# Kernel optimization log

Measured on AMD Instinct MI355X. Metric: run time of the kernel, lower is better.

## Reference

```python
import jax, jax.numpy as jnp
import numpy as np

B, NA, NAA, NPC = 8, 4096, 1024, 4096
K, KNC, G, DA, F, D = 16, 14, 32, 12, 128, 128
NCAT = 38
EPS = 1e-5


def _bgather(x, idx):
    # per-batch fancy gather: x [B, N, ...], idx [B, ...] -> x[b, idx[b]]
    return jax.vmap(lambda a, i: a[i])(x, idx)


def _normalize(v):
    return v / (jnp.linalg.norm(v, axis=-1, keepdims=True) + 1e-8)


def setup_inputs() -> dict:
    key = jax.random.key(0)
    ks = jax.random.split(key, 12)
    return {
        'point_clouds': jax.random.normal(ks[0], (B, NPC, 3), jnp.float32),
        'mask_atom': jnp.ones((B, NA, 1), jnp.float32),
        'mask_aa': jnp.ones((B, NAA, 1), jnp.float32),
        'attr_table': jax.random.normal(ks[1], (NCAT + 1, DA), jnp.float32) * 0.1,
        'gauss_centers': jax.random.normal(ks[2], (G, 3), jnp.float32),
        'W_nem': jax.random.normal(ks[3], (G, DA, F), jnp.float32) / np.sqrt(G * DA),
        'W_att': jax.random.normal(ks[4], (F, D), jnp.float32) / np.sqrt(F),
        'W_feat': jax.random.normal(ks[5], (F, D), jnp.float32) / np.sqrt(F),
        'bn_gamma': jnp.ones((D,), jnp.float32),
        'bn_beta': jnp.zeros((D,), jnp.float32),
        'frame_idx': jax.random.randint(ks[6], (B, NA, 3), 0, NPC),
        'attr_idx': jax.random.randint(ks[7], (B, NA), 0, NCAT + 1),
        'nb_idx': jax.random.randint(ks[8], (B, NA, K), 0, NA),
        'seq_idx_atom': jnp.sort(jax.random.randint(ks[9], (B, NA), 0, NAA), axis=-1),
        'seq_idx_aa': jnp.sort(jax.random.randint(ks[10], (B, NAA), 0, NAA), axis=-1),
        'aa_nb_idx': jax.random.randint(ks[11], (B, NAA, KNC), 0, NA),
    }


def reference(point_clouds, mask_atom, mask_aa, attr_table, gauss_centers,
              W_nem, W_att, W_feat, bn_gamma, bn_beta,
              frame_idx, attr_idx, nb_idx, seq_idx_atom, seq_idx_aa, aa_nb_idx):
    # --- frame builder: local orthonormal frame per atom from 3 gathered points ---
    pts = _bgather(point_clouds, frame_idx)          # [B,NA,3,3]
    center = pts[:, :, 1, :]                         # [B,NA,3]
    u1 = _normalize(pts[:, :, 2, :] - center)
    v = pts[:, :, 0, :] - center
    u2 = _normalize(v - jnp.sum(v * u1, -1, keepdims=True) * u1)
    u3 = jnp.cross(u1, u2)
    R = jnp.stack([u1, u2, u3], axis=-2)             # [B,NA,3,3] rows = axes

    # --- attribute embedding + derived mask (mattr = any nonzero along embed dim) ---
    a = attr_table[attr_idx]                         # [B,NA,DA]
    mattr = jnp.any(a != 0, axis=-1, keepdims=True).astype(a.dtype)
    mask_y = mask_atom * mattr                       # [B,NA,1]

    # --- neighborhood embedding: gather K neighbors, local coords, gaussian basis ---
    c_nb = _bgather(center, nb_idx)                  # [B,NA,K,3]
    rel = jnp.einsum('bnij,bnkj->bnki', R, c_nb - center[:, :, None, :])
    d2 = jnp.sum((rel[:, :, :, None, :] - gauss_centers) ** 2, -1)   # [B,NA,K,G]
    g = jnp.exp(-0.5 * d2)
    a_nb = _bgather(a * mattr, nb_idx)               # [B,NA,K,DA]
    y = jnp.einsum('bnkg,bnka,gaf->bnf', g, a_nb, W_nem) / K          # [B,NA,F]
    y = y * mask_y

    # --- pooling projections (bias-free linears), repeated mask multiplies ---
    att = (y @ W_att) * mask_y                       # [B,NA,D] (one head per channel)
    feat = (y @ W_feat) * mask_y                     # [B,NA,D]

    # --- Neighborhood_Computation: gather 14 atoms per amino acid ---
    att_l = _bgather(att, aa_nb_idx)                 # [B,NAA,KNC,D]
    feat_l = _bgather(feat, aa_nb_idx)               # [B,NAA,KNC,D]
    mask_nb = _bgather(mask_y, aa_nb_idx)            # [B,NAA,KNC,1]
    seq_nb = _bgather(seq_idx_atom, aa_nb_idx)       # [B,NAA,KNC]
    indice_diff = jnp.clip(jnp.abs(seq_nb - seq_idx_aa[:, :, None]), 0, 1).astype(att_l.dtype)
    gate = (1.0 - indice_diff)[..., None]            # pool_mask = 1 - indice_diff

    # --- attention pooling over the 14-neighborhood, gated + masked softmax ---
    logits = jnp.where(mask_nb > 0, att_l, -1e9)
    w = jax.nn.softmax(logits, axis=2) * gate * mask_nb
    w = w / (jnp.sum(w, axis=2, keepdims=True) + 1e-8)
    pooled = jnp.sum(w * feat_l, axis=2) * mask_aa   # [B,NAA,D]

    # --- masked BatchNorm1d over valid aa positions, then ReLU ---
    n = jnp.sum(mask_aa) + 1e-8
    mean = jnp.sum(pooled * mask_aa, (0, 1)) / n
    var = jnp.sum(mask_aa * (pooled - mean) ** 2, (0, 1)) / n
    out = bn_gamma * (pooled - mean) * jax.lax.rsqrt(var + EPS) + bn_beta
    out = jax.nn.relu(out * mask_aa)
    return out, mask_aa
```

## Files before the change

### kernel.cpp

```cpp
#include <hip/hip_runtime.h>
#include <hip/hip_bf16.h>

#define B_    8
#define NA_   4096
#define NAA_  1024
#define NPC_  4096
#define K_    16
#define KNC_  14
#define G_    32
#define DA_   12
#define F_    128
#define D_    128

typedef __attribute__((ext_vector_type(8))) short short8;
typedef __attribute__((ext_vector_type(4))) float floatx4;

__device__ __forceinline__ unsigned short f2bf(float x) {
    __hip_bfloat16 h = __float2bfloat16(x);
    return *reinterpret_cast<unsigned short*>(&h);
}
__device__ __forceinline__ float bf2f(unsigned short u) {
    __hip_bfloat16 h;
    *reinterpret_cast<unsigned short*>(&h) = u;
    return __bfloat162float(h);
}

__global__ __launch_bounds__(256) void k_geom(
    const float* __restrict__ pc,
    const float* __restrict__ mask_atom,
    const float* __restrict__ attr_table,
    const float* __restrict__ gauss,
    const int* __restrict__ frame_idx,
    const int* __restrict__ attr_idx,
    const int* __restrict__ nb_idx,
    const float* __restrict__ W_nem, const float* __restrict__ W_att,
    const float* __restrict__ W_feat,
    unsigned int* __restrict__ Mout,
    float* __restrict__ mask_y,
    unsigned short* __restrict__ WnT,
    unsigned short* __restrict__ W2T)
{
    const int tid = threadIdx.x;

    if (blockIdx.x >= 4096) {
        const int idx = (blockIdx.x - 4096) * 256 + tid;
        if (idx < 128 * 384) {
            const int f = idx / 384, ga = idx % 384;
            WnT[idx] = f2bf(W_nem[(size_t)ga * F_ + f]);
        } else if (idx < 128 * 384 + 256 * 128) {
            const int j = idx - 128 * 384;
            const int n = j / 128, k = j % 128;
            const float v = (n < 128) ? W_att[(size_t)k * F_ + n]
                                      : W_feat[(size_t)k * F_ + (n - 128)];
            W2T[j] = f2bf(v);
        }
        return;
    }

    const int a0 = blockIdx.x * 8;
    const int b  = a0 >> 12;

    __shared__ float  Rs[8][9];
    __shared__ float  cen[8][3];
    __shared__ int    nbs[8][K_];
    __shared__ int    ais[8][K_];
    __shared__ __align__(16) float rel4[8][K_][4];
    __shared__ __align__(16) float anb4[8][K_][12];

    if (tid < 8) {
        const int atom = a0 + tid;
        const int fb = atom * 3;
        const int i0 = frame_idx[fb + 0];
        const int i1 = frame_idx[fb + 1];
        const int i2 = frame_idx[fb + 2];
        const float* pcb = pc + (size_t)b * NPC_ * 3;
        float p0x = pcb[i0*3+0], p0y = pcb[i0*3+1], p0z = pcb[i0*3+2];
        float cx  = pcb[i1*3+0], cy  = pcb[i1*3+1], cz  = pcb[i1*3+2];
        float p2x = pcb[i2*3+0], p2y = pcb[i2*3+1], p2z = pcb[i2*3+2];
        float u1x = p2x - cx, u1y = p2y - cy, u1z = p2z - cz;
        float n1 = sqrtf(u1x*u1x + u1y*u1y + u1z*u1z) + 1e-8f;
        u1x /= n1; u1y /= n1; u1z /= n1;
        float vx = p0x - cx, vy = p0y - cy, vz = p0z - cz;
        float dot = vx*u1x + vy*u1y + vz*u1z;
        float u2x = vx - dot*u1x, u2y = vy - dot*u1y, u2z = vz - dot*u1z;
        float n2 = sqrtf(u2x*u2x + u2y*u2y + u2z*u2z) + 1e-8f;
        u2x /= n2; u2y /= n2; u2z /= n2;
        float u3x = u1y*u2z - u1z*u2y;
        float u3y = u1z*u2x - u1x*u2z;
        float u3z = u1x*u2y - u1y*u2x;
        Rs[tid][0]=u1x; Rs[tid][1]=u1y; Rs[tid][2]=u1z;
        Rs[tid][3]=u2x; Rs[tid][4]=u2y; Rs[tid][5]=u2z;
        Rs[tid][6]=u3x; Rs[tid][7]=u3y; Rs[tid][8]=u3z;
        cen[tid][0]=cx; cen[tid][1]=cy; cen[tid][2]=cz;
        const int ai = attr_idx[atom];
        float m = 0.f;
        #pragma unroll
        for (int a = 0; a < DA_; a++)
            if (attr_table[ai*DA_ + a] != 0.f) m = 1.f;
        mask_y[atom] = mask_atom[atom] * m;
    }
    if (tid < 128) {
        const int t = tid >> 4, k = tid & 15;
        nbs[t][k] = nb_idx[(a0 + t) * K_ + k];
    }
    __syncthreads();

    if (tid < 128) {
        const int t = tid >> 4, k = tid & 15;
        const int j  = nbs[t][k];
        ais[t][k] = attr_idx[b * NA_ + j];
        const int fj = frame_idx[(b * NA_ + j) * 3 + 1];
        const float* pcb = pc + (size_t)b * NPC_ * 3;
        float dx = pcb[fj*3+0] - cen[t][0];
        float dy = pcb[fj*3+1] - cen[t][1];
        float dz = pcb[fj*3+2] - cen[t][2];
        rel4[t][k][0] = Rs[t][0]*dx + Rs[t][1]*dy + Rs[t][2]*dz;
        rel4[t][k][1] = Rs[t][3]*dx + Rs[t][4]*dy + Rs[t][5]*dz;
        rel4[t][k][2] = Rs[t][6]*dx + Rs[t][7]*dy + Rs[t][8]*dz;
        rel4[t][k][3] = 0.f;
    }
    __syncthreads();

    if (tid < 128) {
        const int t = tid >> 4, k = tid & 15;
        const float4* src = (const float4*)attr_table + (size_t)ais[t][k] * 3;
        float4* dst = (float4*)&anb4[t][k][0];
        dst[0] = src[0]; dst[1] = src[1]; dst[2] = src[2];
    }
    __syncthreads();

    {
        const int t = tid >> 5, g = tid & 31;
        const float gx = gauss[g*3+0], gy = gauss[g*3+1], gz = gauss[g*3+2];
        float acc[DA_];
        #pragma unroll
        for (int a = 0; a < DA_; a++) acc[a] = 0.f;
        #pragma unroll
        for (int k = 0; k < K_; k++) {
            const float4 r  = *(const float4*)&rel4[t][k][0];
            const float dx = r.x - gx, dy = r.y - gy, dz = r.z - gz;
            const float gv = __expf(-0.5f * (dx*dx + dy*dy + dz*dz));
            const float4 a0 = *(const float4*)&anb4[t][k][0];
            const float4 a1 = *(const float4*)&anb4[t][k][4];
            const float4 a2 = *(const float4*)&anb4[t][k][8];
            acc[0] += gv*a0.x; acc[1] += gv*a0.y; acc[2] += gv*a0.z; acc[3] += gv*a0.w;
            acc[4] += gv*a1.x; acc[5] += gv*a1.y; acc[6] += gv*a1.z; acc[7] += gv*a1.w;
            acc[8] += gv*a2.x; acc[9] += gv*a2.y; acc[10]+= gv*a2.z; acc[11]+= gv*a2.w;
        }
        const int atom = a0 + t;
        unsigned int* dst = Mout + (size_t)atom * (384/2) + g * 6;
        #pragma unroll
        for (int i = 0; i < 6; i++) {
            const unsigned int lo = f2bf(acc[2*i]);
            const unsigned int hi = f2bf(acc[2*i+1]);
            dst[i] = lo | (hi << 16);
        }
    }
}

__global__ __launch_bounds__(256) void k_gemm(
    const unsigned short* __restrict__ M,
    const unsigned short* __restrict__ WnT,
    const unsigned short* __restrict__ W2T,
    const float* __restrict__ masky,
    unsigned short* __restrict__ AF)
{
    const int mb   = blockIdx.x * 32;
    const int wave = threadIdx.x >> 6, lane = threadIdx.x & 63;
    const int l15  = lane & 15, quad = lane >> 4;

    __shared__ __align__(16) unsigned short Ys[32][136];
    __shared__ float mk[32];

    if (threadIdx.x < 32) mk[threadIdx.x] = masky[mb + threadIdx.x];

    const int n0 = wave * 32;
    const unsigned short* ap0 = M   + (size_t)(mb + l15) * 384 + quad * 8;
    const unsigned short* ap1 = ap0 + (size_t)16 * 384;
    const unsigned short* bp0 = WnT + (size_t)(n0 + l15) * 384 + quad * 8;
    const unsigned short* bp1 = bp0 + (size_t)16 * 384;

    floatx4 c00 = {0.f,0.f,0.f,0.f}, c01 = {0.f,0.f,0.f,0.f};
    floatx4 c10 = {0.f,0.f,0.f,0.f}, c11 = {0.f,0.f,0.f,0.f};
    #pragma unroll
    for (int k0 = 0; k0 < 384; k0 += 32) {
        short8 a0 = *reinterpret_cast<const short8*>(ap0 + k0);
        short8 a1 = *reinterpret_cast<const short8*>(ap1 + k0);
        short8 b0 = *reinterpret_cast<const short8*>(bp0 + k0);
        short8 b1 = *reinterpret_cast<const short8*>(bp1 + k0);
        c00 = __builtin_amdgcn_mfma_f32_16x16x32_bf16(a0, b0, c00, 0, 0, 0);
        c01 = __builtin_amdgcn_mfma_f32_16x16x32_bf16(a0, b1, c01, 0, 0, 0);
        c10 = __builtin_amdgcn_mfma_f32_16x16x32_bf16(a1, b0, c10, 0, 0, 0);
        c11 = __builtin_amdgcn_mfma_f32_16x16x32_bf16(a1, b1, c11, 0, 0, 0);
    }
    __syncthreads();
    #pragma unroll
    for (int r = 0; r < 4; r++) {
        const int r0 = quad * 4 + r;
        const float s0 = mk[r0]      * (1.f / 16.f);
        const float s1 = mk[16 + r0] * (1.f / 16.f);
        Ys[r0][n0 + l15]           = f2bf(c00[r] * s0);
        Ys[r0][n0 + 16 + l15]      = f2bf(c01[r] * s0);
        Ys[16 + r0][n0 + l15]      = f2bf(c10[r] * s1);
        Ys[16 + r0][n0 + 16 + l15] = f2bf(c11[r] * s1);
    }
    __syncthreads();

    const int c0 = wave * 64;
    const unsigned short* bq = W2T + (size_t)(c0 + l15) * F_ + quad * 8;

    floatx4 f0[4], f1[4];
    #pragma unroll
    for (int t = 0; t < 4; t++) {
        f0[t] = (floatx4){0.f,0.f,0.f,0.f};
        f1[t] = (floatx4){0.f,0.f,0.f,0.f};
    }
    #pragma unroll
    for (int k0 = 0; k0 < 128; k0 += 32) {
        short8 a0 = *reinterpret_cast<const short8*>(&Ys[l15][k0 + quad * 8]);
        short8 a1 = *reinterpret_cast<const short8*>(&Ys[16 + l15][k0 + quad * 8]);
        #pragma unroll
        for (int t = 0; t < 4; t++) {
            short8 b = *reinterpret_cast<const short8*>(bq + (size_t)t * 16 * F_ + k0);
            f0[t] = __builtin_amdgcn_mfma_f32_16x16x32_bf16(a0, b, f0[t], 0, 0, 0);
            f1[t] = __builtin_amdgcn_mfma_f32_16x16x32_bf16(a1, b, f1[t], 0, 0, 0);
        }
    }
    #pragma unroll
    for (int r = 0; r < 4; r++) {
        const int r0 = quad * 4 + r;
        const float s0 = mk[r0], s1 = mk[16 + r0];
        unsigned short* o0 = AF + (size_t)(mb + r0) * 256 + c0 + l15;
        unsigned short* o1 = AF + (size_t)(mb + 16 + r0) * 256 + c0 + l15;
        #pragma unroll
        for (int t = 0; t < 4; t++) {
            o0[t * 16] = f2bf(f0[t][r] * s0);
            o1[t * 16] = f2bf(f1[t][r] * s1);
        }
    }
}

__global__ __launch_bounds__(256) void k_pool(
    const unsigned short* __restrict__ AF,
    const float* __restrict__ mask_y,
    const float* __restrict__ mask_aa,
    const int* __restrict__ seq_idx_atom,
    const int* __restrict__ seq_idx_aa,
    const int* __restrict__ aa_nb_idx,
    float* __restrict__ pooled)
{
    const int tid = threadIdx.x;
    const int rl  = tid >> 7;
    const int f   = tid & 127;
    const int row = blockIdx.x * 2 + rl;
    const int b   = row >> 10;

    __shared__ float gateS[2][KNC_], maskS[2][KNC_];
    __shared__ int   jS[2][KNC_];

    if (tid < 2 * KNC_) {
        const int r = tid / KNC_, k = tid % KNC_;
        const int rr = blockIdx.x * 2 + r;
        const int j = aa_nb_idx[rr * KNC_ + k];
        jS[r][k] = j;
        maskS[r][k] = mask_y[(rr >> 10) * NA_ + j];
        const int sa = seq_idx_aa[rr];
        const int sn = seq_idx_atom[(rr >> 10) * NA_ + j];
        gateS[r][k] = (sn == sa) ? 1.f : 0.f;
    }
    __syncthreads();

    float av[KNC_], fv[KNC_];
    #pragma unroll
    for (int k = 0; k < KNC_; k++) {
        const size_t o = ((size_t)(b * NA_ + jS[rl][k])) * 256 + f;
        av[k] = bf2f(AF[o]);
        fv[k] = bf2f(AF[o + 128]);
    }
    float m = -1e30f;
    #pragma unroll
    for (int k = 0; k < KNC_; k++) {
        const float l = (maskS[rl][k] > 0.f) ? av[k] : -1e9f;
        av[k] = l;
        m = fmaxf(m, l);
    }
    float s = 0.f;
    #pragma unroll
    for (int k = 0; k < KNC_; k++) { av[k] = __expf(av[k] - m); s += av[k]; }
    float tot = 0.f, p = 0.f;
    #pragma unroll
    for (int k = 0; k < KNC_; k++) {
        const float w = av[k] / s * gateS[rl][k] * maskS[rl][k];
        tot += w;
        p   += w * fv[k];
    }
    p = p / (tot + 1e-8f);
    p *= mask_aa[row];
    pooled[(size_t)row * F_ + f] = p;
}

__global__ __launch_bounds__(128) void k_stats(
    const float* __restrict__ pooled,
    const float* __restrict__ mask_aa,
    float* __restrict__ stats)
{
    const int tid = threadIdx.x;
    const int r0  = blockIdx.x * 128;
    float s1 = 0.f, s2 = 0.f;
    for (int r = 0; r < 128; r++) {
        const float v = pooled[(size_t)(r0 + r) * F_ + tid];
        s1 += v;
        s2 += v * v;
    }
    atomicAdd(&stats[tid], s1);
    atomicAdd(&stats[F_ + tid], s2);
    if (tid == 0) {
        float n = 0.f;
        for (int r = 0; r < 128; r++) n += mask_aa[r0 + r];
        atomicAdd(&stats[2 * F_], n);
    }
}

__global__ __launch_bounds__(256) void k_final(
    const float* __restrict__ pooled,
    const float* __restrict__ stats,
    const float* __restrict__ gamma,
    const float* __restrict__ beta,
    const float* __restrict__ mask_aa,
    float* __restrict__ out)
{
    const int idx = blockIdx.x * 256 + threadIdx.x;
    const int f   = idx & (D_ - 1);
    const int row = idx >> 7;
    const float n    = stats[2 * F_] + 1e-8f;
    const float mean = stats[f] / n;
    const float var  = stats[F_ + f] / n - mean * mean;
    const float ma   = mask_aa[row];
    float v = gamma[f] * (pooled[idx] - mean) * rsqrtf(var + 1e-5f) + beta[f];
    v = fmaxf(v * ma, 0.f);
    out[idx] = v;
    if (idx < B_ * NAA_) out[B_ * NAA_ * D_ + idx] = mask_aa[idx];
}

extern "C" void kernel_launch(void* const* d_in, const int* in_sizes, int n_in,
                              void* d_out, int out_size, void* d_ws, size_t ws_size,
                              hipStream_t stream) {
    const float* pc         = (const float*)d_in[0];
    const float* mask_atom  = (const float*)d_in[1];
    const float* mask_aa    = (const float*)d_in[2];
    const float* attr_table = (const float*)d_in[3];
    const float* gauss      = (const float*)d_in[4];
    const float* W_nem      = (const float*)d_in[5];
    const float* W_att      = (const float*)d_in[6];
    const float* W_feat     = (const float*)d_in[7];
    const float* gamma      = (const float*)d_in[8];
    const float* beta       = (const float*)d_in[9];
    const int* frame_idx    = (const int*)d_in[10];
    const int* attr_idx     = (const int*)d_in[11];
    const int* nb_idx       = (const int*)d_in[12];
    const int* seq_idx_atom = (const int*)d_in[13];
    const int* seq_idx_aa   = (const int*)d_in[14];
    const int* aa_nb_idx    = (const int*)d_in[15];

    char* base = (char*)d_ws;
    unsigned short* M   = (unsigned short*)base;
    unsigned short* AF  = (unsigned short*)(base + 25165824);
    unsigned short* WnT = (unsigned short*)(base + 25165824 + 16777216);
    unsigned short* W2T = (unsigned short*)(base + 25165824 + 16777216 + 98304);
    float* masky  = (float*)(base + 25165824 + 16777216 + 98304 + 65536);
    float* pooled = (float*)(base + 25165824 + 16777216 + 98304 + 65536 + 131072);
    float* stats  = (float*)(base + 25165824 + 16777216 + 98304 + 65536 + 131072 + 4194304);

    hipMemsetAsync(stats, 0, 257 * sizeof(float), stream);

    k_geom<<<4096 + 320, 256, 0, stream>>>(pc, mask_atom, attr_table, gauss,
                                           frame_idx, attr_idx, nb_idx,
                                           W_nem, W_att, W_feat,
                                           (unsigned int*)M, masky, WnT, W2T);
    k_gemm<<<B_*NA_/32, 256, 0, stream>>>(M, WnT, W2T, masky, AF);
    k_pool<<<B_*NAA_/2, 256, 0, stream>>>(AF, masky, mask_aa,
                                          seq_idx_atom, seq_idx_aa, aa_nb_idx,
                                          pooled);
    k_stats<<<64, 128, 0, stream>>>(pooled, mask_aa, stats);
    k_final<<<(B_*NAA_*D_) / 256, 256, 0, stream>>>(pooled, stats, gamma, beta,
                                                    mask_aa, (float*)d_out);
}
```

Measured before the change: 171.7 us.

## Fuse geometry+GEMM via shared-memory M tile and fold BN stats into pooling

The weight-transpose prep moves into its own small kernel. The geometry/Gaussian-embedding stage is merged with the MFMA GEMM so the 32x384 bf16 M tile stays in LDS instead of round-tripping about 25 MB through global memory. Attribute neighbours are stored as packed bf16 in LDS, and the geometry scratch shares space with the GEMM's Ys buffer. The pooling kernel now handles 8 rows per block and accumulates the BatchNorm sums with a block reduction, which removes the separate serial stats kernel. The risks are lower occupancy from the larger LDS footprint and small precision changes from storing attributes as bf16.

```diff
diff --git a/kernel.cpp b/kernel.cpp
--- a/kernel.cpp
+++ b/kernel.cpp
@@ -24,8 +24,32 @@
     *reinterpret_cast<unsigned short*>(&h) = u;
     return __bfloat162float(h);
 }
-
-__global__ __launch_bounds__(256) void k_geom(
+__device__ __forceinline__ float bflo(unsigned int u) {
+    return __uint_as_float(u << 16);
+}
+__device__ __forceinline__ float bfhi(unsigned int u) {
+    return __uint_as_float(u & 0xffff0000u);
+}
+
+__global__ __launch_bounds__(256) void k_prep(
+    const float* __restrict__ W_nem, const float* __restrict__ W_att,
+    const float* __restrict__ W_feat,
+    unsigned short* __restrict__ WnT, unsigned short* __restrict__ W2T)
+{
+    const int idx = blockIdx.x * 256 + threadIdx.x;
+    if (idx < 128 * 384) {
+        const int f = idx / 384, ga = idx % 384;
+        WnT[idx] = f2bf(W_nem[(size_t)ga * F_ + f]);
+    } else if (idx < 128 * 384 + 256 * 128) {
+        const int j = idx - 128 * 384;
+        const int n = j / 128, k = j % 128;
+        const float v = (n < 128) ? W_att[(size_t)k * F_ + n]
+                                  : W_feat[(size_t)k * F_ + (n - 128)];
+        W2T[j] = f2bf(v);
+    }
+}
+
+__global__ __launch_bounds__(256, 3) void k_fused(
     const float* __restrict__ pc,
     const float* __restrict__ mask_atom,
     const float* __restrict__ attr_table,
@@ -33,41 +57,28 @@
     const int* __restrict__ frame_idx,
     const int* __restrict__ attr_idx,
     const int* __restrict__ nb_idx,
-    const float* __restrict__ W_nem, const float* __restrict__ W_att,
-    const float* __restrict__ W_feat,
-    unsigned int* __restrict__ Mout,
+    const unsigned short* __restrict__ WnT,
+    const unsigned short* __restrict__ W2T,
     float* __restrict__ mask_y,
-    unsigned short* __restrict__ WnT,
-    unsigned short* __restrict__ W2T)
+    unsigned short* __restrict__ AF)
 {
+    const int a0  = blockIdx.x * 32;
+    const int b   = a0 >> 12;
     const int tid = threadIdx.x;
-
-    if (blockIdx.x >= 4096) {
-        const int idx = (blockIdx.x - 4096) * 256 + tid;
-        if (idx < 128 * 384) {
-            const int f = idx / 384, ga = idx % 384;
-            WnT[idx] = f2bf(W_nem[(size_t)ga * F_ + f]);
-        } else if (idx < 128 * 384 + 256 * 128) {
-            const int j = idx - 128 * 384;
-            const int n = j / 128, k = j % 128;
-            const float v = (n < 128) ? W_att[(size_t)k * F_ + n]
-                                      : W_feat[(size_t)k * F_ + (n - 128)];
-            W2T[j] = f2bf(v);
-        }
-        return;
-    }
-
-    const int a0 = blockIdx.x * 8;
-    const int b  = a0 >> 12;
-
-    __shared__ float  Rs[8][9];
-    __shared__ float  cen[8][3];
-    __shared__ int    nbs[8][K_];
-    __shared__ int    ais[8][K_];
-    __shared__ __align__(16) float rel4[8][K_][4];
-    __shared__ __align__(16) float anb4[8][K_][12];
-
-    if (tid < 8) {
+    const int wave = tid >> 6, lane = tid & 63;
+    const int l15 = lane & 15, quad = lane >> 4;
+
+    __shared__ unsigned short Ms[32][392];
+    __shared__ __align__(16) char geo_union[20480];
+    __shared__ float Rs[32][9];
+    __shared__ float cen[32][3];
+    __shared__ float mk[32];
+
+    float4        (*rel4)[K_]    = (float4(*)[K_])geo_union;
+    unsigned int  (*anbP)[K_][6] = (unsigned int(*)[K_][6])(geo_union + 8192);
+    unsigned short(*Ys)[136]     = (unsigned short(*)[136])geo_union;
+
+    if (tid < 32) {
         const int atom = a0 + tid;
         const int fb = atom * 3;
         const int i0 = frame_idx[fb + 0];
@@ -97,58 +108,60 @@
         #pragma unroll
         for (int a = 0; a < DA_; a++)
             if (attr_table[ai*DA_ + a] != 0.f) m = 1.f;
-        mask_y[atom] = mask_atom[atom] * m;
-    }
-    if (tid < 128) {
-        const int t = tid >> 4, k = tid & 15;
-        nbs[t][k] = nb_idx[(a0 + t) * K_ + k];
-    }
-    __syncthreads();
-
-    if (tid < 128) {
-        const int t = tid >> 4, k = tid & 15;
-        const int j  = nbs[t][k];
-        ais[t][k] = attr_idx[b * NA_ + j];
+        const float mv = mask_atom[atom] * m;
+        mk[tid] = mv;
+        mask_y[atom] = mv;
+    }
+    __syncthreads();
+
+    #pragma unroll
+    for (int it = 0; it < 2; it++) {
+        const int idx = tid + it * 256;
+        const int t = idx >> 4, k = idx & 15;
+        const int j  = nb_idx[(a0 + t) * K_ + k];
+        const int ai = attr_idx[b * NA_ + j];
         const int fj = frame_idx[(b * NA_ + j) * 3 + 1];
         const float* pcb = pc + (size_t)b * NPC_ * 3;
         float dx = pcb[fj*3+0] - cen[t][0];
         float dy = pcb[fj*3+1] - cen[t][1];
         float dz = pcb[fj*3+2] - cen[t][2];
-        rel4[t][k][0] = Rs[t][0]*dx + Rs[t][1]*dy + Rs[t][2]*dz;
-        rel4[t][k][1] = Rs[t][3]*dx + Rs[t][4]*dy + Rs[t][5]*dz;
-        rel4[t][k][2] = Rs[t][6]*dx + Rs[t][7]*dy + Rs[t][8]*dz;
-        rel4[t][k][3] = 0.f;
-    }
-    __syncthreads();
-
-    if (tid < 128) {
-        const int t = tid >> 4, k = tid & 15;
-        const float4* src = (const float4*)attr_table + (size_t)ais[t][k] * 3;
-        float4* dst = (float4*)&anb4[t][k][0];
-        dst[0] = src[0]; dst[1] = src[1]; dst[2] = src[2];
-    }
-    __syncthreads();
-
-    {
-        const int t = tid >> 5, g = tid & 31;
+        float4 r;
+        r.x = Rs[t][0]*dx + Rs[t][1]*dy + Rs[t][2]*dz;
+        r.y = Rs[t][3]*dx + Rs[t][4]*dy + Rs[t][5]*dz;
+        r.z = Rs[t][6]*dx + Rs[t][7]*dy + Rs[t][8]*dz;
+        r.w = 0.f;
+        rel4[t][k] = r;
+        const float4* src = (const float4*)attr_table + (size_t)ai * 3;
+        #pragma unroll
+        for (int q = 0; q < 3; q++) {
+            const float4 v = src[q];
+            anbP[t][k][q*2]   = (unsigned int)f2bf(v.x) | ((unsigned int)f2bf(v.y) << 16);
+            anbP[t][k][q*2+1] = (unsigned int)f2bf(v.z) | ((unsigned int)f2bf(v.w) << 16);
+        }
+    }
+    __syncthreads();
+
+    #pragma unroll
+    for (int it = 0; it < 4; it++) {
+        const int idx = tid + it * 256;
+        const int t = idx >> 5, g = idx & 31;
         const float gx = gauss[g*3+0], gy = gauss[g*3+1], gz = gauss[g*3+2];
         float acc[DA_];
         #pragma unroll
         for (int a = 0; a < DA_; a++) acc[a] = 0.f;
         #pragma unroll
         for (int k = 0; k < K_; k++) {
-            const float4 r  = *(const float4*)&rel4[t][k][0];
+            const float4 r = rel4[t][k];
             const float dx = r.x - gx, dy = r.y - gy, dz = r.z - gz;
             const float gv = __expf(-0.5f * (dx*dx + dy*dy + dz*dz));
-            const float4 a0 = *(const float4*)&anb4[t][k][0];
-            const float4 a1 = *(const float4*)&anb4[t][k][4];
-            const float4 a2 = *(const float4*)&anb4[t][k][8];
-            acc[0] += gv*a0.x; acc[1] += gv*a0.y; acc[2] += gv*a0.z; acc[3] += gv*a0.w;
-            acc[4] += gv*a1.x; acc[5] += gv*a1.y; acc[6] += gv*a1.z; acc[7] += gv*a1.w;
-            acc[8] += gv*a2.x; acc[9] += gv*a2.y; acc[10]+= gv*a2.z; acc[11]+= gv*a2.w;
-        }
-        const int atom = a0 + t;
-        unsigned int* dst = Mout + (size_t)atom * (384/2) + g * 6;
+            #pragma unroll
+            for (int q = 0; q < 6; q++) {
+                const unsigned int u = anbP[t][k][q];
+                acc[2*q]   += gv * bflo(u);
+                acc[2*q+1] += gv * bfhi(u);
+            }
+        }
+        unsigned int* dst = (unsigned int*)&Ms[t][g * 12];
         #pragma unroll
         for (int i = 0; i < 6; i++) {
             const unsigned int lo = f2bf(acc[2*i]);
@@ -156,27 +169,9 @@
             dst[i] = lo | (hi << 16);
         }
     }
-}
-
-__global__ __launch_bounds__(256) void k_gemm(
-    const unsigned short* __restrict__ M,
-    const unsigned short* __restrict__ WnT,
-    const unsigned short* __restrict__ W2T,
-    const float* __restrict__ masky,
-    unsigned short* __restrict__ AF)
-{
-    const int mb   = blockIdx.x * 32;
-    const int wave = threadIdx.x >> 6, lane = threadIdx.x & 63;
-    const int l15  = lane & 15, quad = lane >> 4;
-
-    __shared__ __align__(16) unsigned short Ys[32][136];
-    __shared__ float mk[32];
-
-    if (threadIdx.x < 32) mk[threadIdx.x] = masky[mb + threadIdx.x];
+    __syncthreads();
 
     const int n0 = wave * 32;
-    const unsigned short* ap0 = M   + (size_t)(mb + l15) * 384 + quad * 8;
-    const unsigned short* ap1 = ap0 + (size_t)16 * 384;
     const unsigned short* bp0 = WnT + (size_t)(n0 + l15) * 384 + quad * 8;
     const unsigned short* bp1 = bp0 + (size_t)16 * 384;
 
@@ -184,14 +179,14 @@
     floatx4 c10 = {0.f,0.f,0.f,0.f}, c11 = {0.f,0.f,0.f,0.f};
     #pragma unroll
     for (int k0 = 0; k0 < 384; k0 += 32) {
-        short8 a0 = *reinterpret_cast<const short8*>(ap0 + k0);
-        short8 a1 = *reinterpret_cast<const short8*>(ap1 + k0);
+        short8 a0v = *reinterpret_cast<const short8*>(&Ms[l15][quad * 8 + k0]);
+        short8 a1v = *reinterpret_cast<const short8*>(&Ms[16 + l15][quad * 8 + k0]);
         short8 b0 = *reinterpret_cast<const short8*>(bp0 + k0);
         short8 b1 = *reinterpret_cast<const short8*>(bp1 + k0);
-        c00 = __builtin_amdgcn_mfma_f32_16x16x32_bf16(a0, b0, c00, 0, 0, 0);
-        c01 = __builtin_amdgcn_mfma_f32_16x16x32_bf16(a0, b1, c01, 0, 0, 0);
-        c10 = __builtin_amdgcn_mfma_f32_16x16x32_bf16(a1, b0, c10, 0, 0, 0);
-        c11 = __builtin_amdgcn_mfma_f32_16x16x32_bf16(a1, b1, c11, 0, 0, 0);
+        c00 = __builtin_amdgcn_mfma_f32_16x16x32_bf16(a0v, b0, c00, 0, 0, 0);
+        c01 = __builtin_amdgcn_mfma_f32_16x16x32_bf16(a0v, b1, c01, 0, 0, 0);
+        c10 = __builtin_amdgcn_mfma_f32_16x16x32_bf16(a1v, b0, c10, 0, 0, 0);
+        c11 = __builtin_amdgcn_mfma_f32_16x16x32_bf16(a1v, b1, c11, 0, 0, 0);
     }
     __syncthreads();
     #pragma unroll
@@ -217,21 +212,21 @@
     }
     #pragma unroll
     for (int k0 = 0; k0 < 128; k0 += 32) {
-        short8 a0 = *reinterpret_cast<const short8*>(&Ys[l15][k0 + quad * 8]);
-        short8 a1 = *reinterpret_cast<const short8*>(&Ys[16 + l15][k0 + quad * 8]);
+        short8 a0v = *reinterpret_cast<const short8*>(&Ys[l15][k0 + quad * 8]);
+        short8 a1v = *reinterpret_cast<const short8*>(&Ys[16 + l15][k0 + quad * 8]);
         #pragma unroll
         for (int t = 0; t < 4; t++) {
-            short8 b = *reinterpret_cast<const short8*>(bq + (size_t)t * 16 * F_ + k0);
-            f0[t] = __builtin_amdgcn_mfma_f32_16x16x32_bf16(a0, b, f0[t], 0, 0, 0);
-            f1[t] = __builtin_amdgcn_mfma_f32_16x16x32_bf16(a1, b, f1[t], 0, 0, 0);
+            short8 bv = *reinterpret_cast<const short8*>(bq + (size_t)t * 16 * F_ + k0);
+            f0[t] = __builtin_amdgcn_mfma_f32_16x16x32_bf16(a0v, bv, f0[t], 0, 0, 0);
+            f1[t] = __builtin_amdgcn_mfma_f32_16x16x32_bf16(a1v, bv, f1[t], 0, 0, 0);
         }
     }
     #pragma unroll
     for (int r = 0; r < 4; r++) {
         const int r0 = quad * 4 + r;
         const float s0 = mk[r0], s1 = mk[16 + r0];
-        unsigned short* o0 = AF + (size_t)(mb + r0) * 256 + c0 + l15;
-        unsigned short* o1 = AF + (size_t)(mb + 16 + r0) * 256 + c0 + l15;
+        unsigned short* o0 = AF + (size_t)(a0 + r0) * 256 + c0 + l15;
+        unsigned short* o1 = AF + (size_t)(a0 + 16 + r0) * 256 + c0 + l15;
         #pragma unroll
         for (int t = 0; t < 4; t++) {
             o0[t * 16] = f2bf(f0[t][r] * s0);
@@ -240,83 +235,87 @@
     }
 }
 
-__global__ __launch_bounds__(256) void k_pool(
+__global__ __launch_bounds__(256) void k_pool_stats(
     const unsigned short* __restrict__ AF,
     const float* __restrict__ mask_y,
     const float* __restrict__ mask_aa,
     const int* __restrict__ seq_idx_atom,
     const int* __restrict__ seq_idx_aa,
     const int* __restrict__ aa_nb_idx,
-    float* __restrict__ pooled)
+    float* __restrict__ pooled,
+    float* __restrict__ stats)
 {
-    const int tid = threadIdx.x;
-    const int rl  = tid >> 7;
-    const int f   = tid & 127;
-    const int row = blockIdx.x * 2 + rl;
-    const int b   = row >> 10;
-
-    __shared__ float gateS[2][KNC_], maskS[2][KNC_];
-    __shared__ int   jS[2][KNC_];
-
-    if (tid < 2 * KNC_) {
+    const int tid  = threadIdx.x;
+    const int rl   = tid >> 7;
+    const int f    = tid & 127;
+    const int row0 = blockIdx.x * 8;
+
+    __shared__ float gateS[8][KNC_], maskS[8][KNC_];
+    __shared__ int   jS[8][KNC_];
+    __shared__ float red[128];
+
+    if (tid < 8 * KNC_) {
         const int r = tid / KNC_, k = tid % KNC_;
-        const int rr = blockIdx.x * 2 + r;
+        const int rr = row0 + r;
+        const int bb = rr >> 10;
         const int j = aa_nb_idx[rr * KNC_ + k];
         jS[r][k] = j;
-        maskS[r][k] = mask_y[(rr >> 10) * NA_ + j];
+        maskS[r][k] = mask_y[bb * NA_ + j];
         const int sa = seq_idx_aa[rr];
-        const int sn = seq_idx_atom[(rr >> 10) * NA_ + j];
+        const int sn = seq_idx_atom[bb * NA_ + j];
         gateS[r][k] = (sn == sa) ? 1.f : 0.f;
     }
     __syncthreads();
 
-    float av[KNC_], fv[KNC_];
-    #pragma unroll
-    for (int k = 0; k < KNC_; k++) {
-        const size_t o = ((size_t)(b * NA_ + jS[rl][k])) * 256 + f;
-        av[k] = bf2f(AF[o]);
-        fv[k] = bf2f(AF[o + 128]);
-    }
-    float m = -1e30f;
-    #pragma unroll
-    for (int k = 0; k < KNC_; k++) {
-        const float l = (maskS[rl][k] > 0.f) ? av[k] : -1e9f;
-        av[k] = l;
-        m = fmaxf(m, l);
-    }
-    float s = 0.f;
-    #pragma unroll
-    for (int k = 0; k < KNC_; k++) { av[k] = __expf(av[k] - m); s += av[k]; }
-    float tot = 0.f, p = 0.f;
-    #pragma unroll
-    for (int k = 0; k < KNC_; k++) {
-        const float w = av[k] / s * gateS[rl][k] * maskS[rl][k];
-        tot += w;
-        p   += w * fv[k];
-    }
-    p = p / (tot + 1e-8f);
-    p *= mask_aa[row];
-    pooled[(size_t)row * F_ + f] = p;
-}
-
-__global__ __launch_bounds__(128) void k_stats(
-    const float* __restrict__ pooled,
-    const float* __restrict__ mask_aa,
-    float* __restrict__ stats)
-{
-    const int tid = threadIdx.x;
-    const int r0  = blockIdx.x * 128;
     float s1 = 0.f, s2 = 0.f;
-    for (int r = 0; r < 128; r++) {
-        const float v = pooled[(size_t)(r0 + r) * F_ + tid];
-        s1 += v;
-        s2 += v * v;
-    }
-    atomicAdd(&stats[tid], s1);
-    atomicAdd(&stats[F_ + tid], s2);
+    #pragma unroll
+    for (int it = 0; it < 4; it++) {
+        const int r   = it * 2 + rl;
+        const int row = row0 + r;
+        const int bb  = row >> 10;
+
+        float av[KNC_], fv[KNC_];
+        #pragma unroll
+        for (int k = 0; k < KNC_; k++) {
+            const size_t o = ((size_t)(bb * NA_ + jS[r][k])) * 256 + f;
+            av[k] = bf2f(AF[o]);
+            fv[k] = bf2f(AF[o + 128]);
+        }
+        float m = -1e30f;
+        #pragma unroll
+        for (int k = 0; k < KNC_; k++) {
+            const float l = (maskS[r][k] > 0.f) ? av[k] : -1e9f;
+            av[k] = l;
+            m = fmaxf(m, l);
+        }
+        float s = 0.f;
+        #pragma unroll
+        for (int k = 0; k < KNC_; k++) { av[k] = __expf(av[k] - m); s += av[k]; }
+        float tot = 0.f, p = 0.f;
+        #pragma unroll
+        for (int k = 0; k < KNC_; k++) {
+            const float w = av[k] / s * gateS[r][k] * maskS[r][k];
+            tot += w;
+            p   += w * fv[k];
+        }
+        p = p / (tot + 1e-8f);
+        p *= mask_aa[row];
+        pooled[(size_t)row * F_ + f] = p;
+        s1 += p;
+        s2 += p * p;
+    }
+
+    if (rl == 1) red[f] = s1;
+    __syncthreads();
+    if (rl == 0) atomicAdd(&stats[f], s1 + red[f]);
+    __syncthreads();
+    if (rl == 1) red[f] = s2;
+    __syncthreads();
+    if (rl == 0) atomicAdd(&stats[F_ + f], s2 + red[f]);
     if (tid == 0) {
         float n = 0.f;
-        for (int r = 0; r < 128; r++) n += mask_aa[r0 + r];
+        #pragma unroll
+        for (int r = 0; r < 8; r++) n += mask_aa[row0 + r];
         atomicAdd(&stats[2 * F_], n);
     }
 }
@@ -363,25 +362,22 @@
     const int* aa_nb_idx    = (const int*)d_in[15];
 
     char* base = (char*)d_ws;
-    unsigned short* M   = (unsigned short*)base;
-    unsigned short* AF  = (unsigned short*)(base + 25165824);
-    unsigned short* WnT = (unsigned short*)(base + 25165824 + 16777216);
-    unsigned short* W2T = (unsigned short*)(base + 25165824 + 16777216 + 98304);
-    float* masky  = (float*)(base + 25165824 + 16777216 + 98304 + 65536);
-    float* pooled = (float*)(base + 25165824 + 16777216 + 98304 + 65536 + 131072);
-    float* stats  = (float*)(base + 25165824 + 16777216 + 98304 + 65536 + 131072 + 4194304);
+    unsigned short* AF  = (unsigned short*)base;
+    unsigned short* WnT = (unsigned short*)(base + 16777216);
+    unsigned short* W2T = (unsigned short*)(base + 16777216 + 98304);
+    float* masky  = (float*)(base + 16777216 + 98304 + 65536);
+    float* pooled = (float*)(base + 16777216 + 98304 + 65536 + 131072);
+    float* stats  = (float*)(base + 16777216 + 98304 + 65536 + 131072 + 4194304);
 
     hipMemsetAsync(stats, 0, 257 * sizeof(float), stream);
 
-    k_geom<<<4096 + 320, 256, 0, stream>>>(pc, mask_atom, attr_table, gauss,
+    k_prep<<<320, 256, 0, stream>>>(W_nem, W_att, W_feat, WnT, W2T);
+    k_fused<<<B_*NA_/32, 256, 0, stream>>>(pc, mask_atom, attr_table, gauss,
                                            frame_idx, attr_idx, nb_idx,
-                                           W_nem, W_att, W_feat,
-                                           (unsigned int*)M, masky, WnT, W2T);
-    k_gemm<<<B_*NA_/32, 256, 0, stream>>>(M, WnT, W2T, masky, AF);
-    k_pool<<<B_*NAA_/2, 256, 0, stream>>>(AF, masky, mask_aa,
-                                          seq_idx_atom, seq_idx_aa, aa_nb_idx,
-                                          pooled);
-    k_stats<<<64, 128, 0, stream>>>(pooled, mask_aa, stats);
+                                           WnT, W2T, masky, AF);
+    k_pool_stats<<<B_*NAA_/8, 256, 0, stream>>>(AF, masky, mask_aa,
+                                                seq_idx_atom, seq_idx_aa,
+                                                aa_nb_idx, pooled, stats);
     k_final<<<(B_*NAA_*D_) / 256, 256, 0, stream>>>(pooled, stats, gamma, beta,
                                                     mask_aa, (float*)d_out);
 }
```

Result: faster. 166.4 us (-3.1%).
